# Kernel tuning notes

Hardware: AMD Instinct MI355X
Metric: run time of the kernel (lower is better)

## Reference

```python
import jax, jax.numpy as jnp
import numpy as np

N = 100000      # nodes
E = 1600000     # edges (avg degree 16)
G = 64          # graphs in the batch
SIZES = [64, 32, 64, 64]   # GAT layer sizes (num_features=64)
MLP = [64, 32, 10]         # num_classes=10
EPS = 1e-6


def _xavier(key, shape):
    fan_in, fan_out = shape[0], shape[1]
    lim = np.sqrt(6.0 / (fan_in + fan_out)).astype(np.float32)
    return jax.random.uniform(key, shape, jnp.float32, -lim, lim)


def setup_inputs() -> dict:
    key = jax.random.key(0)
    ks = jax.random.split(key, 24)
    inp = {
        'x': jax.random.normal(ks[0], (N, SIZES[0]), jnp.float32),
        'src': jax.random.randint(ks[1], (E,), 0, N, jnp.int32),
        'tgt': jax.random.randint(ks[2], (E,), 0, N, jnp.int32),
        'graph_ids': jax.random.randint(ks[3], (N,), 0, G, jnp.int32),
    }
    k = 4
    for i, (di, do) in enumerate(zip(SIZES[:-1], SIZES[1:])):
        inp[f'fw{i}'] = _xavier(ks[k], (2 * di, do)); k += 1
        inp[f'fb{i}'] = jnp.zeros((do,), jnp.float32)
        inp[f'ww{i}'] = _xavier(ks[k], (2 * di, 1)); k += 1
        inp[f'wb{i}'] = jnp.zeros((1,), jnp.float32)
    for i, (di, do) in enumerate(zip(MLP[:-1], MLP[1:])):
        inp[f'mw{i}'] = _xavier(ks[k], (di, do)); k += 1
        inp[f'mb{i}'] = jnp.zeros((do,), jnp.float32)
    return inp


def _gat_layer(x, src, tgt, fw, fb, ww, wb):
    # gather endpoints and form edge features [E, 2*d_i]
    h = jnp.concatenate([x[src], x[tgt]], axis=1)
    y = jax.nn.relu(h @ fw + fb)          # [E, d_o]
    a = h @ ww + wb                        # [E, 1]
    a_exp = jnp.exp(a - jnp.max(a))        # global-max shift, as in the original
    den = jax.ops.segment_sum(a_exp, tgt, num_segments=N) + EPS   # == Mtgt @ a_exp + eps
    num = jax.ops.segment_sum(y * a_exp, tgt, num_segments=N)     # == Mtgt @ (y*a_exp)
    return num / den                       # [N, d_o]


def reference(x, src, tgt, graph_ids,
              fw0, fb0, ww0, wb0,
              fw1, fb1, ww1, wb1,
              fw2, fb2, ww2, wb2,
              mw0, mb0, mw1, mb1):
    x = _gat_layer(x, src, tgt, fw0, fb0, ww0, wb0)
    x = _gat_layer(x, src, tgt, fw1, fb1, ww1, wb1)
    x = _gat_layer(x, src, tgt, fw2, fb2, ww2, wb2)
    g = jax.ops.segment_sum(x, graph_ids, num_segments=G)   # == Mgraph.T @ x
    g = jax.nn.relu(g @ mw0 + mb0)
    g = g @ mw1 + mb1                      # identity act on last layer
    return g
```

## Files before the change

### kernel.cpp

```cpp
#include <hip/hip_runtime.h>
#include <hip/hip_bf16.h>
#include <math.h>

#define NGRAPH 64
#define EPSV 1e-6f
#define CH 4096

__device__ __forceinline__ unsigned enc_f32(float f){
    unsigned u = __float_as_uint(f);
    return (u & 0x80000000u) ? ~u : (u | 0x80000000u);
}
__device__ __forceinline__ float dec_f32(unsigned u){
    return (u & 0x80000000u) ? __uint_as_float(u & 0x7FFFFFFFu) : __uint_as_float(~u);
}
__device__ __forceinline__ unsigned bf16_rn(float x){
    unsigned u = __float_as_uint(x);
    return (u + 0x7fffu + ((u>>16)&1u)) >> 16;
}
__device__ __forceinline__ float bflo(unsigned u){ return __uint_as_float(u<<16); }
__device__ __forceinline__ float bfhi(unsigned u){ return __uint_as_float(u & 0xffff0000u); }

__global__ __launch_bounds__(256) void k_hist_c(const int* __restrict__ tgt,
                                                int* __restrict__ bhist,
                                                int E, int shift, int nbuk){
    __shared__ int h[256];
    int t = threadIdx.x;
    h[t] = 0; __syncthreads();
    int blk = blockIdx.x;
    int chunk = blk >> 1;
    int base = blk*2048;
    int lim  = base + 2048; if(lim > E) lim = E;
    for(int i=base+t; i<lim; i+=256)
        atomicAdd(&h[tgt[i]>>shift], 1);
    __syncthreads();
    if(t < nbuk && h[t]) atomicAdd(&bhist[chunk*nbuk + t], h[t]);
}

__global__ __launch_bounds__(256) void k_btot(const int* __restrict__ bhist, int* __restrict__ btot,
                                              int nchunk, int nbuk){
    __shared__ int red[256];
    int b = blockIdx.x, t = threadIdx.x;
    int s = 0;
    for(int blk=t; blk<nchunk; blk+=256) s += bhist[blk*nbuk + b];
    red[t] = s; __syncthreads();
    for(int off=128; off>0; off>>=1){
        if(t<off) red[t] += red[t+off];
        __syncthreads();
    }
    if(t==0) btot[b] = red[0];
}

__global__ __launch_bounds__(256) void k_bbase0(const int* __restrict__ btot, int* __restrict__ bbase0, int nbuk){
    __shared__ int s[256];
    int t = threadIdx.x;
    int v = (t<nbuk) ? btot[t] : 0;
    s[t] = v; __syncthreads();
    for(int off=1; off<256; off<<=1){
        int a = (t>=off) ? s[t-off] : 0;
        __syncthreads();
        s[t] += a;
        __syncthreads();
    }
    if(t<nbuk) bbase0[t] = s[t] - v;
}

__global__ __launch_bounds__(512) void k_bbase(const int* __restrict__ bhist, const int* __restrict__ bbase0,
                                               int* __restrict__ bbase, int nchunk, int nbuk){
    __shared__ int s[512];
    int b = blockIdx.x, t = threadIdx.x;
    int v = (t<nchunk) ? bhist[t*nbuk + b] : 0;
    s[t] = v; __syncthreads();
    for(int off=1; off<512; off<<=1){
        int a = (t>=off) ? s[t-off] : 0;
        __syncthreads();
        s[t] += a;
        __syncthreads();
    }
    if(t<nchunk) bbase[t*nbuk + b] = bbase0[b] + s[t] - v;
}

__global__ __launch_bounds__(256) void k_place(const int* __restrict__ src, const int* __restrict__ tgt,
                                               const int* __restrict__ bbase, int2* __restrict__ ebuf,
                                               const float* __restrict__ e1, const float* __restrict__ e2,
                                               unsigned* __restrict__ amax_enc,
                                               int E, int shift, int nbuk){
    __shared__ int lcur[256];
    __shared__ float wm[4];
    int t = threadIdx.x, blk = blockIdx.x;
    lcur[t] = (t<nbuk) ? bbase[blk*nbuk + t] : 0;
    __syncthreads();
    int base = blk*CH;
    int lim  = base + CH; if(lim > E) lim = E;
    float m = 0.f;
    for(int i=base+t; i<lim; i+=256){
        int ss = src[i], tt = tgt[i];
        m = fmaxf(m, e1[ss] * e2[tt]);
        int p = atomicAdd(&lcur[tt>>shift], 1);
        ebuf[p] = make_int2(ss, tt);
    }
    for(int off=32; off>0; off>>=1) m = fmaxf(m, __shfl_xor(m, off));
    if((t&63)==0) wm[t>>6] = m;
    __syncthreads();
    if(t==0){
        float mm = fmaxf(fmaxf(wm[0],wm[1]), fmaxf(wm[2],wm[3]));
        atomicMax(amax_enc, enc_f32(mm));
    }
}

__global__ __launch_bounds__(512) void k_sortb(const int2* __restrict__ ebuf,
                                               const int* __restrict__ bbase0, const int* __restrict__ btot,
                                               int* __restrict__ row_start, int* __restrict__ sorted_src,
                                               int N, int E, int shift, int nbuk){
    __shared__ int sc[512];
    int b = blockIdx.x, t = threadIdx.x;
    int ebeg = bbase0[b];
    int eend = ebeg + btot[b];
    int nbeg = b << shift;
    int nloc = N - nbeg; if(nloc > 512) nloc = 512;
    sc[t] = 0; __syncthreads();
    for(int i=ebeg+t; i<eend; i+=512)
        atomicAdd(&sc[ebuf[i].y - nbeg], 1);
    __syncthreads();
    int v = sc[t];
    for(int off=1; off<512; off<<=1){
        int a = (t>=off) ? sc[t-off] : 0;
        __syncthreads();
        sc[t] += a;
        __syncthreads();
    }
    int pos0 = ebeg + sc[t] - v;
    if(t < nloc) row_start[nbeg + t] = pos0;
    if(b == nbuk-1 && t == 0) row_start[N] = E;
    __syncthreads();
    sc[t] = pos0;
    __syncthreads();
    for(int i=ebeg+t; i<eend; i+=512){
        int2 e = ebuf[i];
        int p = atomicAdd(&sc[e.y - nbeg], 1);
        sorted_src[p] = e.x;
    }
}

template<int DI, int DO>
__global__ __launch_bounds__(256) void k_xform(
    const float* __restrict__ x, const float* __restrict__ fw,
    const float* __restrict__ ww,
    unsigned* __restrict__ ubf, float* __restrict__ v,
    float* __restrict__ e1, float* __restrict__ e2, int N)
{
    constexpr int NSLICE = 2*DO/16;
    constexpr int CP = DO/2;
    int lane = threadIdx.x & 63;
    int wid  = __builtin_amdgcn_readfirstlane(threadIdx.x >> 6);
    int wg   = blockIdx.x*4 + wid;
    int ngroups = (N+63)>>6;
    if(wg >= ngroups*NSLICE) return;
    int slice = wg % NSLICE;
    int group = wg / NSLICE;
    int n  = group*64 + lane;
    bool act = n < N;
    int nn = act ? n : N-1;
    bool uhalf = slice < DO/16;
    int scol = (slice & (DO/16 - 1))*16;
    const float* wp  = fw + (uhalf ? 0 : DI*DO) + scol;
    const float* wwp = ww + (uhalf ? 0 : DI);
    float acc[16];
    #pragma unroll
    for(int j=0;j<16;j++) acc[j]=0.f;
    float p = 0.f;
    #pragma unroll
    for(int k4=0;k4<DI/4;k4++){
        float4 xv = *reinterpret_cast<const float4*>(&x[(size_t)nn*DI + k4*4]);
        #pragma unroll
        for(int kk=0;kk<4;kk++){
            float xk = (kk==0)?xv.x:(kk==1)?xv.y:(kk==2)?xv.z:xv.w;
            int k = k4*4+kk;
            p = fmaf(xk, wwp[k], p);
            #pragma unroll
            for(int j=0;j<16;j++) acc[j] = fmaf(xk, wp[k*DO + j], acc[j]);
        }
    }
    if(act){
        if(uhalf){
            unsigned pk[8];
            #pragma unroll
            for(int j=0;j<8;j++)
                pk[j] = bf16_rn(acc[2*j]) | (bf16_rn(acc[2*j+1])<<16);
            unsigned* dst = &ubf[(size_t)n*CP + scol/2];
            *reinterpret_cast<uint4*>(dst)   = make_uint4(pk[0],pk[1],pk[2],pk[3]);
            *reinterpret_cast<uint4*>(dst+4) = make_uint4(pk[4],pk[5],pk[6],pk[7]);
        } else {
            #pragma unroll
            for(int j4=0;j4<4;j4++)
                *reinterpret_cast<float4*>(&v[(size_t)n*DO + scol + j4*4]) =
                    make_float4(acc[j4*4],acc[j4*4+1],acc[j4*4+2],acc[j4*4+3]);
        }
        if(scol==0) (uhalf ? e1 : e2)[n] = __expf(p);
    }
}

template<int DO, bool DIV>
__global__ __launch_bounds__(256) void k_aggregate2(
    const int* __restrict__ row_start, const int* __restrict__ sorted_src,
    const unsigned* __restrict__ ubf, const float* __restrict__ v,
    const float* __restrict__ e1, const float* __restrict__ e2,
    const float* __restrict__ fb,
    const unsigned* __restrict__ amax_enc,
    float* __restrict__ den_out, float* __restrict__ pmax_out,
    float* __restrict__ xout, int N)
{
    constexpr int CP = DO/2;
    constexpr int PN = 64/CP;
    float epsA = 0.f;
    if(DIV) epsA = EPSV * dec_f32(*amax_enc);
    int lane = threadIdx.x & 63;
    int wid  = threadIdx.x >> 6;
    int c2   = lane & (CP-1);
    int grp  = lane >> (CP==32 ? 5 : 4);
    float fx = fb[2*c2], fy = fb[2*c2+1];
    int gw = blockIdx.x*4 + wid;
    int nwaves = gridDim.x*4;
    for(int n=gw; n<N; n+=nwaves){
        float2 vv = *reinterpret_cast<const float2*>(&v[(size_t)n*DO + 2*c2]);
        float wx = vv.x + fx, wy = vv.y + fy;
        float e2n = e2[n];
        int beg = row_start[n], end = row_start[n+1];
        float ax = 0.f, ay = 0.f, den = 0.f, pm = 0.f;
        int idx = beg + grp;
        for(; idx + 7*PN < end; idx += 8*PN){
            int s_[8]; float e_[8]; unsigned u_[8];
            #pragma unroll
            for(int q=0;q<8;q++) s_[q] = sorted_src[idx+q*PN];
            #pragma unroll
            for(int q=0;q<8;q++){ e_[q] = e1[s_[q]]; u_[q] = ubf[(size_t)s_[q]*CP+c2]; }
            #pragma unroll
            for(int q=0;q<8;q++){
                float p = e_[q]*e2n;
                den += p;
                if(!DIV) pm = fmaxf(pm, p);
                ax = fmaf(p, fmaxf(bflo(u_[q])+wx,0.f), ax);
                ay = fmaf(p, fmaxf(bfhi(u_[q])+wy,0.f), ay);
            }
        }
        for(; idx + 3*PN < end; idx += 4*PN){
            int s_[4]; float e_[4]; unsigned u_[4];
            #pragma unroll
            for(int q=0;q<4;q++) s_[q] = sorted_src[idx+q*PN];
            #pragma unroll
            for(int q=0;q<4;q++){ e_[q] = e1[s_[q]]; u_[q] = ubf[(size_t)s_[q]*CP+c2]; }
            #pragma unroll
            for(int q=0;q<4;q++){
                float p = e_[q]*e2n;
                den += p;
                if(!DIV) pm = fmaxf(pm, p);
                ax = fmaf(p, fmaxf(bflo(u_[q])+wx,0.f), ax);
                ay = fmaf(p, fmaxf(bfhi(u_[q])+wy,0.f), ay);
            }
        }
        for(; idx < end; idx += PN){
            int s = sorted_src[idx];
            float e = e1[s];
            unsigned uu = ubf[(size_t)s*CP+c2];
            float p = e*e2n;
            den += p;
            if(!DIV) pm = fmaxf(pm, p);
            ax = fmaf(p, fmaxf(bflo(uu)+wx,0.f), ax);
            ay = fmaf(p, fmaxf(bfhi(uu)+wy,0.f), ay);
        }
        #pragma unroll
        for(int off=CP; off<64; off<<=1){
            den += __shfl_xor(den, off);
            ax  += __shfl_xor(ax , off);
            ay  += __shfl_xor(ay , off);
            if(!DIV) pm = fmaxf(pm, __shfl_xor(pm, off));
        }
        if(DIV){
            if(lane < CP){
                float d = den + epsA;
                *reinterpret_cast<float2*>(&xout[(size_t)n*DO + 2*c2]) =
                    make_float2(ax/d, ay/d);
            }
        } else {
            if(lane < CP)
                *reinterpret_cast<float2*>(&xout[(size_t)n*DO + 2*c2]) =
                    make_float2(ax, ay);
            if(lane == 0){ den_out[n] = den; pmax_out[n] = pm; }
        }
    }
}

__global__ __launch_bounds__(256) void k_amax(const float* __restrict__ pmax,
                                              unsigned* __restrict__ amax_enc, int N){
    __shared__ float wm[4];
    float m = 0.f;
    for(int i = blockIdx.x*256 + threadIdx.x; i<N; i += gridDim.x*256)
        m = fmaxf(m, pmax[i]);
    for(int off=32; off>0; off>>=1) m = fmaxf(m, __shfl_xor(m, off));
    if((threadIdx.x&63)==0) wm[threadIdx.x>>6] = m;
    __syncthreads();
    if(threadIdx.x==0)
        atomicMax(amax_enc, enc_f32(fmaxf(fmaxf(wm[0],wm[1]), fmaxf(wm[2],wm[3]))));
}

__global__ __launch_bounds__(256) void k_div(float* __restrict__ x, const float* __restrict__ den,
                                             const unsigned* __restrict__ amax_enc, int N){
    float epsA = EPSV * dec_f32(*amax_enc);
    int tot = N*16;
    int i = blockIdx.x*256 + threadIdx.x;
    int stride = gridDim.x*256;
    float4* xp = reinterpret_cast<float4*>(x);
    for(; i<tot; i+=stride){
        int n = i>>4;
        float r = 1.f/(den[n] + epsA);
        float4 t = xp[i];
        t.x*=r; t.y*=r; t.z*=r; t.w*=r;
        xp[i] = t;
    }
}

__global__ __launch_bounds__(512) void k_pool1(const float* __restrict__ x, const int* __restrict__ gid,
                                               float* __restrict__ gpart, int N){
    __shared__ float bins[64*64];
    int t = threadIdx.x;
    for(int i=t;i<4096;i+=512) bins[i]=0.f;
    __syncthreads();
    int lane = t & 63, wid = t>>6;
    int gw = blockIdx.x*8 + wid;
    int nwaves = gridDim.x*8;
    for(int n=gw; n<N; n+=nwaves){
        int gi = gid[n];
        atomicAdd(&bins[gi*64 + lane], x[(size_t)n*64 + lane]);
    }
    __syncthreads();
    float* dst = &gpart[(size_t)blockIdx.x*4096];
    for(int i=t;i<4096;i+=512) dst[i] = bins[i];
}

__global__ __launch_bounds__(256) void k_pool2(const float* __restrict__ gpart, float* __restrict__ g, int nblk){
    int i = blockIdx.x*256 + threadIdx.x;
    float s0=0.f, s1=0.f, s2=0.f, s3=0.f;
    int k=0;
    for(; k+3<nblk; k+=4){
        s0 += gpart[(size_t)k*4096+i];
        s1 += gpart[(size_t)(k+1)*4096+i];
        s2 += gpart[(size_t)(k+2)*4096+i];
        s3 += gpart[(size_t)(k+3)*4096+i];
    }
    for(; k<nblk; k++) s0 += gpart[(size_t)k*4096+i];
    g[i] = (s0+s1)+(s2+s3);
}

__global__ __launch_bounds__(1024) void k_mlp(const float* __restrict__ g,
        const float* __restrict__ mw0, const float* __restrict__ mb0,
        const float* __restrict__ mw1, const float* __restrict__ mb1,
        float* __restrict__ out){
    __shared__ float lg[64*64];
    __shared__ float hid[64*32];
    int t = threadIdx.x;
    for(int i=t;i<4096;i+=1024) lg[i]=g[i];
    __syncthreads();
    for(int i=t;i<2048;i+=1024){
        int r = i>>5, h = i&31;
        float a = mb0[h];
        for(int k=0;k<64;k++) a = fmaf(lg[r*64+k], mw0[k*32+h], a);
        hid[i] = fmaxf(a, 0.f);
    }
    __syncthreads();
    for(int i=t;i<640;i+=1024){
        int r = i/10, j = i%10;
        float a = mb1[j];
        for(int h=0;h<32;h++) a = fmaf(hid[r*32+h], mw1[h*10+j], a);
        out[i] = a;
    }
}

extern "C" void kernel_launch(void* const* d_in, const int* in_sizes, int n_in,
                              void* d_out, int out_size, void* d_ws, size_t ws_size,
                              hipStream_t stream){
    const float* x   = (const float*)d_in[0];
    const int*   src = (const int*)d_in[1];
    const int*   tgt = (const int*)d_in[2];
    const int*   gid = (const int*)d_in[3];
    const float* fw[3] = {(const float*)d_in[4],  (const float*)d_in[8],  (const float*)d_in[12]};
    const float* fb[3] = {(const float*)d_in[5],  (const float*)d_in[9],  (const float*)d_in[13]};
    const float* ww[3] = {(const float*)d_in[6],  (const float*)d_in[10], (const float*)d_in[14]};
    const float* mw0 = (const float*)d_in[16];
    const float* mb0 = (const float*)d_in[17];
    const float* mw1 = (const float*)d_in[18];
    const float* mb1 = (const float*)d_in[19];
    float* out = (float*)d_out;

    const int N = in_sizes[3];
    const int E = in_sizes[1];
    const int NG = (N + 63)/64;
    const int NCHUNK = (E + CH - 1)/CH;
    const int NPOOL = 512;
    int shift = 0;
    while(((N-1)>>shift) >= 256) shift++;
    const int nbuk = ((N-1)>>shift) + 1;

    char* ws = (char*)d_ws;
    size_t off = 0;
    auto alloc = [&](size_t bytes)->char*{
        char* p = ws + off;
        off += (bytes + 255) & ~(size_t)255;
        return p;
    };
    int*      row_start  = (int*)     alloc((size_t)(N+1)*4);
    int*      sorted_src = (int*)     alloc((size_t)E*4);
    int2*     ebuf       = (int2*)    alloc((size_t)E*8);
    float*    e1         = (float*)   alloc((size_t)N*4);
    float*    e2         = (float*)   alloc((size_t)N*4);
    float*    den        = (float*)   alloc((size_t)N*4);
    float*    pmax       = (float*)   alloc((size_t)N*4);
    unsigned* ubf        = (unsigned*)alloc((size_t)N*32*4);
    float*    v          = (float*)   alloc((size_t)N*64*4);
    float*    xA         = (float*)   alloc((size_t)N*64*4);
    float*    xB         = (float*)   alloc((size_t)N*64*4);
    unsigned* amax       = (unsigned*)alloc(3*4);
    float*    g          = (float*)   alloc(4096*4);
    float*    gpart      = (float*)   alloc((size_t)NPOOL*4096*4);
    int*      bhist      = (int*)     alloc((size_t)NCHUNK*nbuk*4);
    int*      btot       = (int*)     alloc(256*4);
    int*      bbase0     = (int*)     alloc(256*4);
    int*      bbase      = (int*)     alloc((size_t)NCHUNK*nbuk*4);

    hipMemsetAsync(amax,  0, 12, stream);
    hipMemsetAsync(bhist, 0, (size_t)NCHUNK*nbuk*4, stream);

    k_xform<64,32><<<(NG*4+3)/4,256,0,stream>>>(x, fw[0], ww[0], ubf, v, e1, e2, N);

    k_hist_c <<<NCHUNK*2,256,0,stream>>>(tgt, bhist, E, shift, nbuk);
    k_btot   <<<nbuk,256,0,stream>>>(bhist, btot, NCHUNK, nbuk);
    k_bbase0 <<<1,   256,0,stream>>>(btot, bbase0, nbuk);
    k_bbase  <<<nbuk,512,0,stream>>>(bhist, bbase0, bbase, NCHUNK, nbuk);
    k_place  <<<NCHUNK,256,0,stream>>>(src, tgt, bbase, ebuf, e1, e2, &amax[0], E, shift, nbuk);
    k_sortb  <<<nbuk,512,0,stream>>>(ebuf, bbase0, btot, row_start, sorted_src, N, E, shift, nbuk);

    k_aggregate2<32,true><<<2048,256,0,stream>>>(row_start, sorted_src, ubf, v, e1, e2, fb[0],
                                                 &amax[0], nullptr, nullptr, xA, N);
    k_xform<32,64><<<(NG*8+3)/4,256,0,stream>>>(xA, fw[1], ww[1], ubf, v, e1, e2, N);
    k_aggregate2<64,false><<<2048,256,0,stream>>>(row_start, sorted_src, ubf, v, e1, e2, fb[1],
                                                  &amax[1], den, pmax, xB, N);
    k_amax<<<128,256,0,stream>>>(pmax, &amax[1], N);
    k_div <<<2048,256,0,stream>>>(xB, den, &amax[1], N);
    k_xform<64,64><<<(NG*8+3)/4,256,0,stream>>>(xB, fw[2], ww[2], ubf, v, e1, e2, N);
    k_aggregate2<64,false><<<2048,256,0,stream>>>(row_start, sorted_src, ubf, v, e1, e2, fb[2],
                                                  &amax[2], den, pmax, xA, N);
    k_amax<<<128,256,0,stream>>>(pmax, &amax[2], N);
    k_div <<<2048,256,0,stream>>>(xA, den, &amax[2], N);

    k_pool1<<<NPOOL,512,0,stream>>>(xA, gid, gpart, N);
    k_pool2<<<16,  256,0,stream>>>(gpart, g, NPOOL);
    k_mlp  <<<1,  1024,0,stream>>>(g, mw0, mb0, mw1, mb1, out);
}
```

Baseline: 404.4 us.

## Fuse max reduction and division into neighbours; pack edge buffer into one word

The per-node max is now reduced inside the aggregate kernel, with one atomicMax per wave, which removes the pmax buffer and the k_amax launches. The normalization divide is folded into the next layer's xform input load and into the pooling kernel, so the separate k_div passes over the feature matrix disappear. The sort's edge buffer packs src and the local tgt offset into a single 32-bit word, halving its traffic. Packing assumes src<<shift fits in 32 bits, and reusing den across layer 2 and 3 depends on launch ordering.

```diff
diff --git a/kernel.cpp b/kernel.cpp
--- a/kernel.cpp
+++ b/kernel.cpp
@@ -80,7 +80,7 @@
 }
 
 __global__ __launch_bounds__(256) void k_place(const int* __restrict__ src, const int* __restrict__ tgt,
-                                               const int* __restrict__ bbase, int2* __restrict__ ebuf,
+                                               const int* __restrict__ bbase, unsigned* __restrict__ ebuf,
                                                const float* __restrict__ e1, const float* __restrict__ e2,
                                                unsigned* __restrict__ amax_enc,
                                                int E, int shift, int nbuk){
@@ -89,6 +89,7 @@
     int t = threadIdx.x, blk = blockIdx.x;
     lcur[t] = (t<nbuk) ? bbase[blk*nbuk + t] : 0;
     __syncthreads();
+    unsigned msk = (1u<<shift) - 1u;
     int base = blk*CH;
     int lim  = base + CH; if(lim > E) lim = E;
     float m = 0.f;
@@ -96,7 +97,7 @@
         int ss = src[i], tt = tgt[i];
         m = fmaxf(m, e1[ss] * e2[tt]);
         int p = atomicAdd(&lcur[tt>>shift], 1);
-        ebuf[p] = make_int2(ss, tt);
+        ebuf[p] = ((unsigned)ss << shift) | ((unsigned)tt & msk);
     }
     for(int off=32; off>0; off>>=1) m = fmaxf(m, __shfl_xor(m, off));
     if((t&63)==0) wm[t>>6] = m;
@@ -107,7 +108,7 @@
     }
 }
 
-__global__ __launch_bounds__(512) void k_sortb(const int2* __restrict__ ebuf,
+__global__ __launch_bounds__(512) void k_sortb(const unsigned* __restrict__ ebuf,
                                                const int* __restrict__ bbase0, const int* __restrict__ btot,
                                                int* __restrict__ row_start, int* __restrict__ sorted_src,
                                                int N, int E, int shift, int nbuk){
@@ -116,10 +117,11 @@
     int ebeg = bbase0[b];
     int eend = ebeg + btot[b];
     int nbeg = b << shift;
+    unsigned msk = (1u<<shift) - 1u;
     int nloc = N - nbeg; if(nloc > 512) nloc = 512;
     sc[t] = 0; __syncthreads();
     for(int i=ebeg+t; i<eend; i+=512)
-        atomicAdd(&sc[ebuf[i].y - nbeg], 1);
+        atomicAdd(&sc[ebuf[i] & msk], 1);
     __syncthreads();
     int v = sc[t];
     for(int off=1; off<512; off<<=1){
@@ -135,18 +137,19 @@
     sc[t] = pos0;
     __syncthreads();
     for(int i=ebeg+t; i<eend; i+=512){
-        int2 e = ebuf[i];
-        int p = atomicAdd(&sc[e.y - nbeg], 1);
-        sorted_src[p] = e.x;
-    }
-}
-
-template<int DI, int DO>
+        unsigned w = ebuf[i];
+        int p = atomicAdd(&sc[w & msk], 1);
+        sorted_src[p] = (int)(w >> shift);
+    }
+}
+
+template<int DI, int DO, bool FDIV>
 __global__ __launch_bounds__(256) void k_xform(
     const float* __restrict__ x, const float* __restrict__ fw,
     const float* __restrict__ ww,
     unsigned* __restrict__ ubf, float* __restrict__ v,
-    float* __restrict__ e1, float* __restrict__ e2, int N)
+    float* __restrict__ e1, float* __restrict__ e2,
+    const float* __restrict__ den, const unsigned* __restrict__ amax_enc, int N)
 {
     constexpr int NSLICE = 2*DO/16;
     constexpr int CP = DO/2;
@@ -164,6 +167,8 @@
     int scol = (slice & (DO/16 - 1))*16;
     const float* wp  = fw + (uhalf ? 0 : DI*DO) + scol;
     const float* wwp = ww + (uhalf ? 0 : DI);
+    float r = 1.f;
+    if(FDIV) r = 1.f/(den[nn] + EPSV*dec_f32(*amax_enc));
     float acc[16];
     #pragma unroll
     for(int j=0;j<16;j++) acc[j]=0.f;
@@ -171,6 +176,7 @@
     #pragma unroll
     for(int k4=0;k4<DI/4;k4++){
         float4 xv = *reinterpret_cast<const float4*>(&x[(size_t)nn*DI + k4*4]);
+        if(FDIV){ xv.x*=r; xv.y*=r; xv.z*=r; xv.w*=r; }
         #pragma unroll
         for(int kk=0;kk<4;kk++){
             float xk = (kk==0)?xv.x:(kk==1)?xv.y:(kk==2)?xv.z:xv.w;
@@ -205,8 +211,8 @@
     const unsigned* __restrict__ ubf, const float* __restrict__ v,
     const float* __restrict__ e1, const float* __restrict__ e2,
     const float* __restrict__ fb,
-    const unsigned* __restrict__ amax_enc,
-    float* __restrict__ den_out, float* __restrict__ pmax_out,
+    unsigned* __restrict__ amax_enc,
+    float* __restrict__ den_out,
     float* __restrict__ xout, int N)
 {
     constexpr int CP = DO/2;
@@ -220,6 +226,7 @@
     float fx = fb[2*c2], fy = fb[2*c2+1];
     int gw = blockIdx.x*4 + wid;
     int nwaves = gridDim.x*4;
+    float gm = 0.f;
     for(int n=gw; n<N; n+=nwaves){
         float2 vv = *reinterpret_cast<const float2*>(&v[(size_t)n*DO + 2*c2]);
         float wx = vv.x + fx, wy = vv.y + fy;
@@ -284,43 +291,18 @@
             if(lane < CP)
                 *reinterpret_cast<float2*>(&xout[(size_t)n*DO + 2*c2]) =
                     make_float2(ax, ay);
-            if(lane == 0){ den_out[n] = den; pmax_out[n] = pm; }
-        }
-    }
-}
-
-__global__ __launch_bounds__(256) void k_amax(const float* __restrict__ pmax,
-                                              unsigned* __restrict__ amax_enc, int N){
-    __shared__ float wm[4];
-    float m = 0.f;
-    for(int i = blockIdx.x*256 + threadIdx.x; i<N; i += gridDim.x*256)
-        m = fmaxf(m, pmax[i]);
-    for(int off=32; off>0; off>>=1) m = fmaxf(m, __shfl_xor(m, off));
-    if((threadIdx.x&63)==0) wm[threadIdx.x>>6] = m;
-    __syncthreads();
-    if(threadIdx.x==0)
-        atomicMax(amax_enc, enc_f32(fmaxf(fmaxf(wm[0],wm[1]), fmaxf(wm[2],wm[3]))));
-}
-
-__global__ __launch_bounds__(256) void k_div(float* __restrict__ x, const float* __restrict__ den,
-                                             const unsigned* __restrict__ amax_enc, int N){
-    float epsA = EPSV * dec_f32(*amax_enc);
-    int tot = N*16;
-    int i = blockIdx.x*256 + threadIdx.x;
-    int stride = gridDim.x*256;
-    float4* xp = reinterpret_cast<float4*>(x);
-    for(; i<tot; i+=stride){
-        int n = i>>4;
-        float r = 1.f/(den[n] + epsA);
-        float4 t = xp[i];
-        t.x*=r; t.y*=r; t.z*=r; t.w*=r;
-        xp[i] = t;
-    }
+            if(lane == 0) den_out[n] = den;
+            gm = fmaxf(gm, pm);
+        }
+    }
+    if(!DIV && lane == 0) atomicMax(amax_enc, enc_f32(gm));
 }
 
 __global__ __launch_bounds__(512) void k_pool1(const float* __restrict__ x, const int* __restrict__ gid,
+                                               const float* __restrict__ den, const unsigned* __restrict__ amax_enc,
                                                float* __restrict__ gpart, int N){
     __shared__ float bins[64*64];
+    float epsA = EPSV * dec_f32(*amax_enc);
     int t = threadIdx.x;
     for(int i=t;i<4096;i+=512) bins[i]=0.f;
     __syncthreads();
@@ -329,7 +311,8 @@
     int nwaves = gridDim.x*8;
     for(int n=gw; n<N; n+=nwaves){
         int gi = gid[n];
-        atomicAdd(&bins[gi*64 + lane], x[(size_t)n*64 + lane]);
+        float r = 1.f/(den[n] + epsA);
+        atomicAdd(&bins[gi*64 + lane], x[(size_t)n*64 + lane]*r);
     }
     __syncthreads();
     float* dst = &gpart[(size_t)blockIdx.x*4096];
@@ -408,11 +391,10 @@
     };
     int*      row_start  = (int*)     alloc((size_t)(N+1)*4);
     int*      sorted_src = (int*)     alloc((size_t)E*4);
-    int2*     ebuf       = (int2*)    alloc((size_t)E*8);
+    unsigned* ebuf       = (unsigned*)alloc((size_t)E*4);
     float*    e1         = (float*)   alloc((size_t)N*4);
     float*    e2         = (float*)   alloc((size_t)N*4);
     float*    den        = (float*)   alloc((size_t)N*4);
-    float*    pmax       = (float*)   alloc((size_t)N*4);
     unsigned* ubf        = (unsigned*)alloc((size_t)N*32*4);
     float*    v          = (float*)   alloc((size_t)N*64*4);
     float*    xA         = (float*)   alloc((size_t)N*64*4);
@@ -428,7 +410,7 @@
     hipMemsetAsync(amax,  0, 12, stream);
     hipMemsetAsync(bhist, 0, (size_t)NCHUNK*nbuk*4, stream);
 
-    k_xform<64,32><<<(NG*4+3)/4,256,0,stream>>>(x, fw[0], ww[0], ubf, v, e1, e2, N);
+    k_xform<64,32,false><<<(NG*4+3)/4,256,0,stream>>>(x, fw[0], ww[0], ubf, v, e1, e2, nullptr, nullptr, N);
 
     k_hist_c <<<NCHUNK*2,256,0,stream>>>(tgt, bhist, E, shift, nbuk);
     k_btot   <<<nbuk,256,0,stream>>>(bhist, btot, NCHUNK, nbuk);
@@ -438,19 +420,15 @@
     k_sortb  <<<nbuk,512,0,stream>>>(ebuf, bbase0, btot, row_start, sorted_src, N, E, shift, nbuk);
 
     k_aggregate2<32,true><<<2048,256,0,stream>>>(row_start, sorted_src, ubf, v, e1, e2, fb[0],
-                                                 &amax[0], nullptr, nullptr, xA, N);
-    k_xform<32,64><<<(NG*8+3)/4,256,0,stream>>>(xA, fw[1], ww[1], ubf, v, e1, e2, N);
+                                                 &amax[0], nullptr, xA, N);
+    k_xform<32,64,false><<<(NG*8+3)/4,256,0,stream>>>(xA, fw[1], ww[1], ubf, v, e1, e2, nullptr, nullptr, N);
     k_aggregate2<64,false><<<2048,256,0,stream>>>(row_start, sorted_src, ubf, v, e1, e2, fb[1],
-                                                  &amax[1], den, pmax, xB, N);
-    k_amax<<<128,256,0,stream>>>(pmax, &amax[1], N);
-    k_div <<<2048,256,0,stream>>>(xB, den, &amax[1], N);
-    k_xform<64,64><<<(NG*8+3)/4,256,0,stream>>>(xB, fw[2], ww[2], ubf, v, e1, e2, N);
+                                                  &amax[1], den, xB, N);
+    k_xform<64,64,true><<<(NG*8+3)/4,256,0,stream>>>(xB, fw[2], ww[2], ubf, v, e1, e2, den, &amax[1], N);
     k_aggregate2<64,false><<<2048,256,0,stream>>>(row_start, sorted_src, ubf, v, e1, e2, fb[2],
-                                                  &amax[2], den, pmax, xA, N);
-    k_amax<<<128,256,0,stream>>>(pmax, &amax[2], N);
-    k_div <<<2048,256,0,stream>>>(xA, den, &amax[2], N);
-
-    k_pool1<<<NPOOL,512,0,stream>>>(xA, gid, gpart, N);
+                                                  &amax[2], den, xA, N);
+
+    k_pool1<<<NPOOL,512,0,stream>>>(xA, gid, den, &amax[2], gpart, N);
     k_pool2<<<16,  256,0,stream>>>(gpart, g, NPOOL);
     k_mlp  <<<1,  1024,0,stream>>>(g, mw0, mb0, mw1, mb1, out);
 }
```

New measurement: 551.0 us. 1.36x slower.
